# Kernel tuning notes

Measured on AMD Instinct MI355X. Metric: run time of the kernel, lower is better.

The kernel has to match this reference:

```python
import jax, jax.numpy as jnp
import numpy as np

B = 64
H = 768  # hidden_dim; x is [B, H, H], split along dim 1 into Q, D of [B, H//2, H]


def setup_inputs() -> dict:
    key = jax.random.key(0)
    kx, kw, kb = jax.random.split(key, 3)
    x = jax.random.normal(kx, (B, H, H), dtype=jnp.float32)
    # nn.Linear(H, H): weight [out, in], bias [out]
    W = jax.random.normal(kw, (H, H), dtype=jnp.float32) * (1.0 / np.sqrt(H))
    b = jax.random.normal(kb, (H,), dtype=jnp.float32) * 0.01
    return {"x": x, "W": W, "b": b}


def reference(x, W, b):
    T = H // 2
    Q = x[:, :T, :]          # [B, T, H]
    D = x[:, T:2 * T, :]     # [B, T, H]
    # Q = tanh(Linear(Q)); torch Linear: y = x @ W^T + b
    Q = jnp.tanh(jnp.einsum('bth,oh->bto', Q, W) + b)  # [B, T, H]
    D_t = jnp.swapaxes(D, 1, 2)                         # [B, H, T]
    L = jnp.einsum('bth,bsh->bts', Q, D)                # [B, T, T]
    A_Q = jnp.swapaxes(jax.nn.softmax(L, axis=1), 1, 2) # softmax over dim 1, then transpose -> [B, T, T]
    C_Q = jnp.matmul(D_t, A_Q)                          # [B, H, T]
    Q_t = jnp.swapaxes(Q, 1, 2)                         # [B, H, T]
    A_D = jax.nn.softmax(L, axis=2)                     # [B, T, T]
    C_D = jnp.matmul(jnp.concatenate((Q_t, C_Q), axis=1), A_D)  # [B, 2H, T]
    C_D_t = jnp.swapaxes(C_D, 1, 2)                     # [B, T, 2H]
    return jnp.concatenate((C_D_t, D), axis=2)          # [B, T, 3H]
```

## Files before the change

kernel.cpp:

```cpp
#include <hip/hip_runtime.h>


typedef __bf16 bf16x8 __attribute__((ext_vector_type(8)));
typedef __bf16 bf16x4 __attribute__((ext_vector_type(4)));
typedef float  f32x4  __attribute__((ext_vector_type(4)));

#define HH 768
#define TT 384

__device__ inline void split8(const float* __restrict__ p, bf16x8& hi, bf16x8& lo) {
    float4 f0 = *(const float4*)p;
    float4 f1 = *(const float4*)(p + 4);
    float f[8] = {f0.x, f0.y, f0.z, f0.w, f1.x, f1.y, f1.z, f1.w};
#pragma unroll
    for (int i = 0; i < 8; i++) {
        __bf16 h = (__bf16)f[i];
        hi[i] = h;
        lo[i] = (__bf16)(f[i] - (float)h);
    }
}

__device__ inline void split8r(float4 f0, float4 f1, bf16x8& hi, bf16x8& lo) {
    float f[8] = {f0.x, f0.y, f0.z, f0.w, f1.x, f1.y, f1.z, f1.w};
#pragma unroll
    for (int i = 0; i < 8; i++) {
        __bf16 h = (__bf16)f[i];
        hi[i] = h;
        lo[i] = (__bf16)(f[i] - (float)h);
    }
}

__device__ inline void gload16(const void* g, void* l) {
    __builtin_amdgcn_global_load_lds(
        (const __attribute__((address_space(1))) unsigned int*)g,
        (__attribute__((address_space(3))) unsigned int*)l, 16, 0, 0);
}

__global__ void prep_kernel(const float* __restrict__ x, __bf16* __restrict__ Dt,
                            float* __restrict__ out) {
    __shared__ float tile[32][33];
    int b = blockIdx.z;
    int h0 = blockIdx.x * 32, s0 = blockIdx.y * 32;
    int tx = threadIdx.x, ty = threadIdx.y;
    const float* src = x + ((size_t)b * HH + TT) * HH;
    float* outb = out + (size_t)b * TT * 2304;
#pragma unroll
    for (int j = 0; j < 4; j++) {
        int s = s0 + ty + 8 * j, h = h0 + tx;
        float v = src[(size_t)s * HH + h];
        tile[ty + 8 * j][tx] = v;
        outb[(size_t)s * 2304 + 1536 + h] = v;
    }
    __syncthreads();
    __bf16* Dtb = Dt + (size_t)b * HH * TT;
#pragma unroll
    for (int j = 0; j < 4; j++) {
        int h = h0 + ty + 8 * j, s = s0 + tx;
        Dtb[(size_t)h * TT + s] = (__bf16)tile[tx][ty + 8 * j];
    }
}

__global__ void splitW_kernel(const float* __restrict__ W, __bf16* __restrict__ Whi,
                              __bf16* __restrict__ Wlo) {
    int idx = blockIdx.x * 256 + threadIdx.x;
    bf16x8 h, l;
    split8(W + (size_t)idx * 8, h, l);
    *(bf16x8*)&Whi[(size_t)idx * 8] = h;
    *(bf16x8*)&Wlo[(size_t)idx * 8] = l;
}

__global__ __launch_bounds__(256) void gemm1_kernel(
    const float* __restrict__ x, const __bf16* __restrict__ Whi,
    const __bf16* __restrict__ Wlo, const float* __restrict__ bias,
    __bf16* __restrict__ Qhi, __bf16* __restrict__ Qlo, __bf16* __restrict__ M4) {
    __shared__ __bf16 Ah[128 * 32], Al[128 * 32];
    __shared__ __bf16 Bh[2][128 * 32], Bl[2][128 * 32];
    const int id = blockIdx.x;
    const int xcd = id & 7, kk = id >> 3;
    const int nb = kk % 6, p = (kk / 6) * 8 + xcd;
    const int mb = p % 3, b = p / 3;
    const int m_blk = mb * 128, n_blk = nb * 128;
    const int tid = threadIdx.x, lane = tid & 63, wave = tid >> 6;
    const int wm = wave >> 1, wn = wave & 1;
    const int r15 = lane & 15, quad = lane >> 4;
    const float* Abase = x + (size_t)b * HH * HH;
    const int ra0 = tid >> 2, qa = tid & 3;
    const float* aptr0 = Abase + (size_t)(m_blk + ra0) * HH + qa * 8;
    const float* aptr1 = Abase + (size_t)(m_blk + ra0 + 64) * HH + qa * 8;
    f32x4 acc[4][4];
#pragma unroll
    for (int i = 0; i < 4; i++)
#pragma unroll
        for (int j = 0; j < 4; j++) acc[i][j] = (f32x4){0.f, 0.f, 0.f, 0.f};

    float4 a00 = *(const float4*)(aptr0);
    float4 a01 = *(const float4*)(aptr0 + 4);
    float4 a10 = *(const float4*)(aptr1);
    float4 a11 = *(const float4*)(aptr1 + 4);
#pragma unroll
    for (int it = 0; it < 2; it++) {
        int c = it * 256 + tid, r = c >> 2, q = c & 3;
        gload16(Whi + (size_t)(n_blk + r) * HH + q * 8, &Bh[0][c * 8]);
        gload16(Wlo + (size_t)(n_blk + r) * HH + q * 8, &Bl[0][c * 8]);
    }
    int cur = 0;
    for (int k0 = 0; k0 < HH; k0 += 32) {
        {
            bf16x8 h, l;
            split8r(a00, a01, h, l);
            *(bf16x8*)&Ah[tid * 8] = h;
            *(bf16x8*)&Al[tid * 8] = l;
            split8r(a10, a11, h, l);
            *(bf16x8*)&Ah[(256 + tid) * 8] = h;
            *(bf16x8*)&Al[(256 + tid) * 8] = l;
        }
        __syncthreads();
        if (k0 + 32 < HH) {
            a00 = *(const float4*)(aptr0 + k0 + 32);
            a01 = *(const float4*)(aptr0 + k0 + 36);
            a10 = *(const float4*)(aptr1 + k0 + 32);
            a11 = *(const float4*)(aptr1 + k0 + 36);
#pragma unroll
            for (int it = 0; it < 2; it++) {
                int c = it * 256 + tid, r = c >> 2, q = c & 3;
                gload16(Whi + (size_t)(n_blk + r) * HH + k0 + 32 + q * 8, &Bh[cur ^ 1][c * 8]);
                gload16(Wlo + (size_t)(n_blk + r) * HH + k0 + 32 + q * 8, &Bl[cur ^ 1][c * 8]);
            }
        }
        bf16x8 ah[4], al[4], bh[4], bl[4];
#pragma unroll
        for (int i = 0; i < 4; i++) {
            int ra = (wm * 64 + i * 16 + r15) * 32 + quad * 8;
            ah[i] = *(const bf16x8*)&Ah[ra];
            al[i] = *(const bf16x8*)&Al[ra];
            int rb = (wn * 64 + i * 16 + r15) * 32 + quad * 8;
            bh[i] = *(const bf16x8*)&Bh[cur][rb];
            bl[i] = *(const bf16x8*)&Bl[cur][rb];
        }
#pragma unroll
        for (int i = 0; i < 4; i++)
#pragma unroll
            for (int j = 0; j < 4; j++) {
                acc[i][j] = __builtin_amdgcn_mfma_f32_16x16x32_bf16(ah[i], bh[j], acc[i][j], 0, 0, 0);
                acc[i][j] = __builtin_amdgcn_mfma_f32_16x16x32_bf16(ah[i], bl[j], acc[i][j], 0, 0, 0);
                acc[i][j] = __builtin_amdgcn_mfma_f32_16x16x32_bf16(al[i], bh[j], acc[i][j], 0, 0, 0);
            }
        __syncthreads();
        cur ^= 1;
    }
    __bf16* Qh = Qhi + (size_t)b * TT * HH;
    __bf16* Ql = Qlo + (size_t)b * TT * HH;
    __bf16* Mb = M4 + (size_t)b * 1536 * TT;
#pragma unroll
    for (int j = 0; j < 4; j++) {
        int col = n_blk + wn * 64 + j * 16 + r15;
        float bv = bias[col];
#pragma unroll
        for (int i = 0; i < 4; i++) {
            int row0 = m_blk + wm * 64 + i * 16 + quad * 4;
            bf16x4 mrow;
#pragma unroll
            for (int r = 0; r < 4; r++) {
                float v = tanhf(acc[i][j][r] + bv);
                __bf16 qh = (__bf16)v;
                Qh[(size_t)(row0 + r) * HH + col] = qh;
                Ql[(size_t)(row0 + r) * HH + col] = (__bf16)(v - (float)qh);
                mrow[r] = qh;
            }
            *(bf16x4*)&Mb[(size_t)col * TT + row0] = mrow;
        }
    }
}

__global__ __launch_bounds__(256) void gemm2_kernel(
    const __bf16* __restrict__ Qhi, const __bf16* __restrict__ Qlo,
    const float* __restrict__ x, float* __restrict__ L) {
    __shared__ __bf16 Ah[2][128 * 32], Al[2][128 * 32];
    __shared__ __bf16 Bh[128 * 32], Bl[128 * 32];
    const int id = blockIdx.x;
    const int xcd = id & 7, kk = id >> 3;
    const int inner = kk % 9, b = (kk / 9) * 8 + xcd;
    const int mb = inner / 3, nb = inner % 3;
    const int m_blk = mb * 128, n_blk = nb * 128;
    const int tid = threadIdx.x, lane = tid & 63, wave = tid >> 6;
    const int wm = wave >> 1, wn = wave & 1;
    const int r15 = lane & 15, quad = lane >> 4;
    const __bf16* Qh = Qhi + (size_t)b * TT * HH;
    const __bf16* Ql = Qlo + (size_t)b * TT * HH;
    const float* Dbase = x + ((size_t)b * HH + TT) * HH;
    const int rb0 = tid >> 2, qb = tid & 3;
    const float* dptr0 = Dbase + (size_t)(n_blk + rb0) * HH + qb * 8;
    const float* dptr1 = Dbase + (size_t)(n_blk + rb0 + 64) * HH + qb * 8;
    f32x4 acc[4][4];
#pragma unroll
    for (int i = 0; i < 4; i++)
#pragma unroll
        for (int j = 0; j < 4; j++) acc[i][j] = (f32x4){0.f, 0.f, 0.f, 0.f};

    float4 d00 = *(const float4*)(dptr0);
    float4 d01 = *(const float4*)(dptr0 + 4);
    float4 d10 = *(const float4*)(dptr1);
    float4 d11 = *(const float4*)(dptr1 + 4);
#pragma unroll
    for (int it = 0; it < 2; it++) {
        int c = it * 256 + tid, r = c >> 2, q = c & 3;
        gload16(Qh + (size_t)(m_blk + r) * HH + q * 8, &Ah[0][c * 8]);
        gload16(Ql + (size_t)(m_blk + r) * HH + q * 8, &Al[0][c * 8]);
    }
    int cur = 0;
    for (int k0 = 0; k0 < HH; k0 += 32) {
        {
            bf16x8 h, l;
            split8r(d00, d01, h, l);
            *(bf16x8*)&Bh[tid * 8] = h;
            *(bf16x8*)&Bl[tid * 8] = l;
            split8r(d10, d11, h, l);
            *(bf16x8*)&Bh[(256 + tid) * 8] = h;
            *(bf16x8*)&Bl[(256 + tid) * 8] = l;
        }
        __syncthreads();
        if (k0 + 32 < HH) {
            d00 = *(const float4*)(dptr0 + k0 + 32);
            d01 = *(const float4*)(dptr0 + k0 + 36);
            d10 = *(const float4*)(dptr1 + k0 + 32);
            d11 = *(const float4*)(dptr1 + k0 + 36);
#pragma unroll
            for (int it = 0; it < 2; it++) {
                int c = it * 256 + tid, r = c >> 2, q = c & 3;
                gload16(Qh + (size_t)(m_blk + r) * HH + k0 + 32 + q * 8, &Ah[cur ^ 1][c * 8]);
                gload16(Ql + (size_t)(m_blk + r) * HH + k0 + 32 + q * 8, &Al[cur ^ 1][c * 8]);
            }
        }
        bf16x8 ah[4], al[4], bh[4], bl[4];
#pragma unroll
        for (int i = 0; i < 4; i++) {
            int ra = (wm * 64 + i * 16 + r15) * 32 + quad * 8;
            ah[i] = *(const bf16x8*)&Ah[cur][ra];
            al[i] = *(const bf16x8*)&Al[cur][ra];
            int rb = (wn * 64 + i * 16 + r15) * 32 + quad * 8;
            bh[i] = *(const bf16x8*)&Bh[rb];
            bl[i] = *(const bf16x8*)&Bl[rb];
        }
#pragma unroll
        for (int i = 0; i < 4; i++)
#pragma unroll
            for (int j = 0; j < 4; j++) {
                acc[i][j] = __builtin_amdgcn_mfma_f32_16x16x32_bf16(ah[i], bh[j], acc[i][j], 0, 0, 0);
                acc[i][j] = __builtin_amdgcn_mfma_f32_16x16x32_bf16(ah[i], bl[j], acc[i][j], 0, 0, 0);
                acc[i][j] = __builtin_amdgcn_mfma_f32_16x16x32_bf16(al[i], bh[j], acc[i][j], 0, 0, 0);
            }
        __syncthreads();
        cur ^= 1;
    }
    float* Lb = L + (size_t)b * TT * TT;
#pragma unroll
    for (int j = 0; j < 4; j++) {
        int col = n_blk + wn * 64 + j * 16 + r15;
#pragma unroll
        for (int i = 0; i < 4; i++) {
            int row0 = m_blk + wm * 64 + i * 16 + quad * 4;
#pragma unroll
            for (int r = 0; r < 4; r++) Lb[(size_t)(row0 + r) * TT + col] = acc[i][j][r];
        }
    }
}

__global__ void softmax_col_kernel(const float* __restrict__ L, __bf16* __restrict__ AQt) {
    int b = blockIdx.y;
    int tx = threadIdx.x, ty = threadIdx.y;
    int s = blockIdx.x * 64 + tx;
    const float* Lb = L + (size_t)b * TT * TT;
    __shared__ float red[4][64];
    float mx = -1e30f;
    for (int t = ty; t < TT; t += 4) mx = fmaxf(mx, Lb[(size_t)t * TT + s]);
    red[ty][tx] = mx;
    __syncthreads();
    mx = fmaxf(fmaxf(red[0][tx], red[1][tx]), fmaxf(red[2][tx], red[3][tx]));
    float sum = 0.f;
    for (int t = ty; t < TT; t += 4) sum += __expf(Lb[(size_t)t * TT + s] - mx);
    __syncthreads();
    red[ty][tx] = sum;
    __syncthreads();
    float inv = 1.0f / (red[0][tx] + red[1][tx] + red[2][tx] + red[3][tx]);
    __bf16* Ab = AQt + (size_t)b * TT * TT;
    for (int t = ty; t < TT; t += 4)
        Ab[(size_t)t * TT + s] = (__bf16)(__expf(Lb[(size_t)t * TT + s] - mx) * inv);
}

__global__ void softmax_row_kernel(const float* __restrict__ L, __bf16* __restrict__ ADt) {
    int b = blockIdx.y;
    int t0 = blockIdx.x * 64;
    int tx = threadIdx.x, ty = threadIdx.y;
    int tid = ty * 64 + tx;
    const float* Lb = L + (size_t)b * TT * TT;
    __shared__ __bf16 ex[64][TT];
    for (int rr = ty; rr < 64; rr += 4) {
        const float* row = Lb + (size_t)(t0 + rr) * TT;
        float v[6];
        float mx = -1e30f;
#pragma unroll
        for (int k = 0; k < 6; k++) {
            v[k] = row[tx + 64 * k];
            mx = fmaxf(mx, v[k]);
        }
#pragma unroll
        for (int off = 32; off > 0; off >>= 1) mx = fmaxf(mx, __shfl_xor(mx, off));
        float sum = 0.f;
#pragma unroll
        for (int k = 0; k < 6; k++) {
            v[k] = __expf(v[k] - mx);
            sum += v[k];
        }
#pragma unroll
        for (int off = 32; off > 0; off >>= 1) sum += __shfl_xor(sum, off);
        float inv = 1.0f / sum;
#pragma unroll
        for (int k = 0; k < 6; k++) ex[rr][tx + 64 * k] = (__bf16)(v[k] * inv);
    }
    __syncthreads();
    __bf16* Ab = ADt + (size_t)b * TT * TT;
    for (int s = tid; s < TT; s += 256) {
#pragma unroll
        for (int j = 0; j < 8; j++) {
            bf16x8 t8;
#pragma unroll
            for (int e = 0; e < 8; e++) t8[e] = ex[j * 8 + e][s];
            *(bf16x8*)&Ab[(size_t)s * TT + t0 + j * 8] = t8;
        }
    }
}

__global__ __launch_bounds__(256) void gemm3_kernel(
    const __bf16* __restrict__ Dt, const __bf16* __restrict__ AQt,
    __bf16* __restrict__ M4) {
    __shared__ __bf16 As[128 * 32], Bs[128 * 32];
    const int id = blockIdx.x;
    const int xcd = id & 7, kk = id >> 3;
    const int inner = kk % 18, b = (kk / 18) * 8 + xcd;
    const int nb = inner % 3, mb = inner / 3;
    const int m_blk = mb * 128, n_blk = nb * 128;
    const int tid = threadIdx.x, lane = tid & 63, wave = tid >> 6;
    const int wm = wave >> 1, wn = wave & 1;
    const int r15 = lane & 15, quad = lane >> 4;
    const __bf16* Ab = Dt + (size_t)b * HH * TT;
    const __bf16* Bb = AQt + (size_t)b * TT * TT;
    f32x4 acc[4][4];
#pragma unroll
    for (int i = 0; i < 4; i++)
#pragma unroll
        for (int j = 0; j < 4; j++) acc[i][j] = (f32x4){0.f, 0.f, 0.f, 0.f};

    for (int k0 = 0; k0 < TT; k0 += 32) {
#pragma unroll
        for (int it = 0; it < 2; it++) {
            int c = it * 256 + tid;
            int r = c >> 2, q = c & 3;
            gload16(Ab + (size_t)(m_blk + r) * TT + k0 + q * 8, &As[c * 8]);
            gload16(Bb + (size_t)(n_blk + r) * TT + k0 + q * 8, &Bs[c * 8]);
        }
        __syncthreads();
        bf16x8 a[4], bf[4];
#pragma unroll
        for (int i = 0; i < 4; i++) {
            a[i] = *(const bf16x8*)&As[(wm * 64 + i * 16 + r15) * 32 + quad * 8];
            bf[i] = *(const bf16x8*)&Bs[(wn * 64 + i * 16 + r15) * 32 + quad * 8];
        }
#pragma unroll
        for (int i = 0; i < 4; i++)
#pragma unroll
            for (int j = 0; j < 4; j++)
                acc[i][j] = __builtin_amdgcn_mfma_f32_16x16x32_bf16(a[i], bf[j], acc[i][j], 0, 0, 0);
        __syncthreads();
    }
    __bf16* Mb = M4 + (size_t)b * 1536 * TT;
#pragma unroll
    for (int j = 0; j < 4; j++) {
        int col = n_blk + wn * 64 + j * 16 + r15;
#pragma unroll
        for (int i = 0; i < 4; i++) {
            int row0 = m_blk + wm * 64 + i * 16 + quad * 4;
#pragma unroll
            for (int r = 0; r < 4; r++)
                Mb[(size_t)(768 + row0 + r) * TT + col] = (__bf16)acc[i][j][r];
        }
    }
}

__global__ __launch_bounds__(256) void gemm4_kernel(
    const __bf16* __restrict__ ADt, const __bf16* __restrict__ M4,
    float* __restrict__ out) {
    __shared__ __bf16 As[128 * 32], Bs[128 * 32];
    const int id = blockIdx.x;
    const int xcd = id & 7, kk = id >> 3;
    const int inner = kk % 36, b = (kk / 36) * 8 + xcd;
    const int nb = inner % 12, mb = inner / 12;
    const int m_blk = mb * 128, n_blk = nb * 128;
    const int tid = threadIdx.x, lane = tid & 63, wave = tid >> 6;
    const int wm = wave >> 1, wn = wave & 1;
    const int r15 = lane & 15, quad = lane >> 4;
    const __bf16* Ab = ADt + (size_t)b * TT * TT;
    const __bf16* Bb = M4 + (size_t)b * 1536 * TT;
    f32x4 acc[4][4];
#pragma unroll
    for (int i = 0; i < 4; i++)
#pragma unroll
        for (int j = 0; j < 4; j++) acc[i][j] = (f32x4){0.f, 0.f, 0.f, 0.f};

    for (int k0 = 0; k0 < TT; k0 += 32) {
#pragma unroll
        for (int it = 0; it < 2; it++) {
            int c = it * 256 + tid;
            int r = c >> 2, q = c & 3;
            gload16(Ab + (size_t)(m_blk + r) * TT + k0 + q * 8, &As[c * 8]);
            gload16(Bb + (size_t)(n_blk + r) * TT + k0 + q * 8, &Bs[c * 8]);
        }
        __syncthreads();
        bf16x8 a[4], bf[4];
#pragma unroll
        for (int i = 0; i < 4; i++) {
            a[i] = *(const bf16x8*)&As[(wm * 64 + i * 16 + r15) * 32 + quad * 8];
            bf[i] = *(const bf16x8*)&Bs[(wn * 64 + i * 16 + r15) * 32 + quad * 8];
        }
#pragma unroll
        for (int i = 0; i < 4; i++)
#pragma unroll
            for (int j = 0; j < 4; j++)
                acc[i][j] = __builtin_amdgcn_mfma_f32_16x16x32_bf16(a[i], bf[j], acc[i][j], 0, 0, 0);
        __syncthreads();
    }
    float* outb = out + (size_t)b * TT * 2304;
#pragma unroll
    for (int j = 0; j < 4; j++) {
        int col = n_blk + wn * 64 + j * 16 + r15;
#pragma unroll
        for (int i = 0; i < 4; i++) {
            int row0 = m_blk + wm * 64 + i * 16 + quad * 4;
#pragma unroll
            for (int r = 0; r < 4; r++)
                outb[(size_t)(row0 + r) * 2304 + col] = acc[i][j][r];
        }
    }
}

extern "C" void kernel_launch(void* const* d_in, const int* in_sizes, int n_in,
                              void* d_out, int out_size, void* d_ws, size_t ws_size,
                              hipStream_t stream) {
    const float* x = (const float*)d_in[0];
    const float* W = (const float*)d_in[1];
    const float* bias = (const float*)d_in[2];
    float* out = (float*)d_out;
    char* ws = (char*)d_ws;

    __bf16* Qhi = (__bf16*)(ws + 0);
    __bf16* Qlo = (__bf16*)(ws + 37748736);
    __bf16* M4 = (__bf16*)(ws + 75497472);
    __bf16* Dt = (__bf16*)(ws + 150994944);
    float* L = (float*)(ws + 188743680);
    __bf16* AQt = (__bf16*)(ws + 0);
    __bf16* ADt = (__bf16*)(ws + 37748736);
    __bf16* Whi = (__bf16*)(ws + 188743680);
    __bf16* Wlo = Whi + 768 * 768;

    prep_kernel<<<dim3(24, 12, 64), dim3(32, 8), 0, stream>>>(x, Dt, out);
    splitW_kernel<<<288, 256, 0, stream>>>(W, Whi, Wlo);
    gemm1_kernel<<<1152, 256, 0, stream>>>(x, Whi, Wlo, bias, Qhi, Qlo, M4);
    gemm2_kernel<<<576, 256, 0, stream>>>(Qhi, Qlo, x, L);
    softmax_col_kernel<<<dim3(6, 64), dim3(64, 4), 0, stream>>>(L, AQt);
    softmax_row_kernel<<<dim3(6, 64), dim3(64, 4), 0, stream>>>(L, ADt);
    gemm3_kernel<<<1152, 256, 0, stream>>>(Dt, AQt, M4);
    gemm4_kernel<<<2304, 256, 0, stream>>>(ADt, M4, out);
}
```

Before: 753.0 us.

## Merge prep into gemm1 launch and fuse both softmax kernels

Folds the D-transpose/copy prep work into the gemm1 launch as extra blocks appended after the GEMM blocks. It also merges the column and row softmax kernels into one launch that dispatches on block index. Together these cut two kernel launches and let independent work share the GPU. The gemm1 block-to-XCD swizzle is dropped in favour of a plain linear mapping, and both kernels now use a larger unified shared buffer, which may lower occupancy for the small prep and softmax blocks.

```diff
diff --git a/kernel.cpp b/kernel.cpp
--- a/kernel.cpp
+++ b/kernel.cpp
@@ -34,30 +34,6 @@
     __builtin_amdgcn_global_load_lds(
         (const __attribute__((address_space(1))) unsigned int*)g,
         (__attribute__((address_space(3))) unsigned int*)l, 16, 0, 0);
-}
-
-__global__ void prep_kernel(const float* __restrict__ x, __bf16* __restrict__ Dt,
-                            float* __restrict__ out) {
-    __shared__ float tile[32][33];
-    int b = blockIdx.z;
-    int h0 = blockIdx.x * 32, s0 = blockIdx.y * 32;
-    int tx = threadIdx.x, ty = threadIdx.y;
-    const float* src = x + ((size_t)b * HH + TT) * HH;
-    float* outb = out + (size_t)b * TT * 2304;
-#pragma unroll
-    for (int j = 0; j < 4; j++) {
-        int s = s0 + ty + 8 * j, h = h0 + tx;
-        float v = src[(size_t)s * HH + h];
-        tile[ty + 8 * j][tx] = v;
-        outb[(size_t)s * 2304 + 1536 + h] = v;
-    }
-    __syncthreads();
-    __bf16* Dtb = Dt + (size_t)b * HH * TT;
-#pragma unroll
-    for (int j = 0; j < 4; j++) {
-        int h = h0 + ty + 8 * j, s = s0 + tx;
-        Dtb[(size_t)h * TT + s] = (__bf16)tile[tx][ty + 8 * j];
-    }
 }
 
 __global__ void splitW_kernel(const float* __restrict__ W, __bf16* __restrict__ Whi,
@@ -69,18 +45,45 @@
     *(bf16x8*)&Wlo[(size_t)idx * 8] = l;
 }
 
-__global__ __launch_bounds__(256) void gemm1_kernel(
+__global__ __launch_bounds__(256) void fused_g1prep_kernel(
     const float* __restrict__ x, const __bf16* __restrict__ Whi,
     const __bf16* __restrict__ Wlo, const float* __restrict__ bias,
-    __bf16* __restrict__ Qhi, __bf16* __restrict__ Qlo, __bf16* __restrict__ M4) {
-    __shared__ __bf16 Ah[128 * 32], Al[128 * 32];
-    __shared__ __bf16 Bh[2][128 * 32], Bl[2][128 * 32];
+    __bf16* __restrict__ Qhi, __bf16* __restrict__ Qlo, __bf16* __restrict__ M4,
+    __bf16* __restrict__ Dt, float* __restrict__ out) {
+    __shared__ __align__(16) char smem[49152];
+    const int tid = threadIdx.x;
+    if (blockIdx.x >= 1152) {
+        float (*tile)[33] = (float(*)[33])smem;
+        int pid = blockIdx.x - 1152;
+        int hb = pid % 24, sb = (pid / 24) % 12, b = pid / 288;
+        int h0 = hb * 32, s0 = sb * 32;
+        int tx = tid & 31, ty = tid >> 5;
+        const float* src = x + ((size_t)b * HH + TT) * HH;
+        float* outb = out + (size_t)b * TT * 2304;
+#pragma unroll
+        for (int j = 0; j < 4; j++) {
+            int s = s0 + ty + 8 * j, h = h0 + tx;
+            float v = src[(size_t)s * HH + h];
+            tile[ty + 8 * j][tx] = v;
+            outb[(size_t)s * 2304 + 1536 + h] = v;
+        }
+        __syncthreads();
+        __bf16* Dtb = Dt + (size_t)b * HH * TT;
+#pragma unroll
+        for (int j = 0; j < 4; j++) {
+            int h = h0 + ty + 8 * j, s = s0 + tx;
+            Dtb[(size_t)h * TT + s] = (__bf16)tile[tx][ty + 8 * j];
+        }
+        return;
+    }
+    __bf16* Ah = (__bf16*)smem;
+    __bf16* Al = (__bf16*)(smem + 8192);
+    __bf16* Bh0 = (__bf16*)(smem + 16384);
+    __bf16* Bl0 = (__bf16*)(smem + 32768);
     const int id = blockIdx.x;
-    const int xcd = id & 7, kk = id >> 3;
-    const int nb = kk % 6, p = (kk / 6) * 8 + xcd;
-    const int mb = p % 3, b = p / 3;
+    const int nb = id % 6, mb = (id / 6) % 3, b = id / 18;
     const int m_blk = mb * 128, n_blk = nb * 128;
-    const int tid = threadIdx.x, lane = tid & 63, wave = tid >> 6;
+    const int lane = tid & 63, wave = tid >> 6;
     const int wm = wave >> 1, wn = wave & 1;
     const int r15 = lane & 15, quad = lane >> 4;
     const float* Abase = x + (size_t)b * HH * HH;
@@ -100,8 +103,8 @@
 #pragma unroll
     for (int it = 0; it < 2; it++) {
         int c = it * 256 + tid, r = c >> 2, q = c & 3;
-        gload16(Whi + (size_t)(n_blk + r) * HH + q * 8, &Bh[0][c * 8]);
-        gload16(Wlo + (size_t)(n_blk + r) * HH + q * 8, &Bl[0][c * 8]);
+        gload16(Whi + (size_t)(n_blk + r) * HH + q * 8, Bh0 + c * 8);
+        gload16(Wlo + (size_t)(n_blk + r) * HH + q * 8, Bl0 + c * 8);
     }
     int cur = 0;
     for (int k0 = 0; k0 < HH; k0 += 32) {
@@ -123,8 +126,10 @@
 #pragma unroll
             for (int it = 0; it < 2; it++) {
                 int c = it * 256 + tid, r = c >> 2, q = c & 3;
-                gload16(Whi + (size_t)(n_blk + r) * HH + k0 + 32 + q * 8, &Bh[cur ^ 1][c * 8]);
-                gload16(Wlo + (size_t)(n_blk + r) * HH + k0 + 32 + q * 8, &Bl[cur ^ 1][c * 8]);
+                gload16(Whi + (size_t)(n_blk + r) * HH + k0 + 32 + q * 8,
+                        Bh0 + (cur ^ 1) * 4096 + c * 8);
+                gload16(Wlo + (size_t)(n_blk + r) * HH + k0 + 32 + q * 8,
+                        Bl0 + (cur ^ 1) * 4096 + c * 8);
             }
         }
         bf16x8 ah[4], al[4], bh[4], bl[4];
@@ -134,8 +139,8 @@
             ah[i] = *(const bf16x8*)&Ah[ra];
             al[i] = *(const bf16x8*)&Al[ra];
             int rb = (wn * 64 + i * 16 + r15) * 32 + quad * 8;
-            bh[i] = *(const bf16x8*)&Bh[cur][rb];
-            bl[i] = *(const bf16x8*)&Bl[cur][rb];
+            bh[i] = *(const bf16x8*)&Bh0[cur * 4096 + rb];
+            bl[i] = *(const bf16x8*)&Bl0[cur * 4096 + rb];
         }
 #pragma unroll
         for (int i = 0; i < 4; i++)
@@ -265,67 +270,66 @@
     }
 }
 
-__global__ void softmax_col_kernel(const float* __restrict__ L, __bf16* __restrict__ AQt) {
+__global__ void sm_fused_kernel(const float* __restrict__ L, __bf16* __restrict__ AQt,
+                                __bf16* __restrict__ ADt) {
+    __shared__ __align__(16) char smem[49152];
     int b = blockIdx.y;
     int tx = threadIdx.x, ty = threadIdx.y;
-    int s = blockIdx.x * 64 + tx;
     const float* Lb = L + (size_t)b * TT * TT;
-    __shared__ float red[4][64];
-    float mx = -1e30f;
-    for (int t = ty; t < TT; t += 4) mx = fmaxf(mx, Lb[(size_t)t * TT + s]);
-    red[ty][tx] = mx;
-    __syncthreads();
-    mx = fmaxf(fmaxf(red[0][tx], red[1][tx]), fmaxf(red[2][tx], red[3][tx]));
-    float sum = 0.f;
-    for (int t = ty; t < TT; t += 4) sum += __expf(Lb[(size_t)t * TT + s] - mx);
-    __syncthreads();
-    red[ty][tx] = sum;
-    __syncthreads();
-    float inv = 1.0f / (red[0][tx] + red[1][tx] + red[2][tx] + red[3][tx]);
-    __bf16* Ab = AQt + (size_t)b * TT * TT;
-    for (int t = ty; t < TT; t += 4)
-        Ab[(size_t)t * TT + s] = (__bf16)(__expf(Lb[(size_t)t * TT + s] - mx) * inv);
-}
-
-__global__ void softmax_row_kernel(const float* __restrict__ L, __bf16* __restrict__ ADt) {
-    int b = blockIdx.y;
-    int t0 = blockIdx.x * 64;
-    int tx = threadIdx.x, ty = threadIdx.y;
-    int tid = ty * 64 + tx;
-    const float* Lb = L + (size_t)b * TT * TT;
-    __shared__ __bf16 ex[64][TT];
-    for (int rr = ty; rr < 64; rr += 4) {
-        const float* row = Lb + (size_t)(t0 + rr) * TT;
-        float v[6];
+    if (blockIdx.x < 6) {
+        float (*red)[64] = (float(*)[64])smem;
+        int s = blockIdx.x * 64 + tx;
         float mx = -1e30f;
-#pragma unroll
-        for (int k = 0; k < 6; k++) {
-            v[k] = row[tx + 64 * k];
-            mx = fmaxf(mx, v[k]);
-        }
-#pragma unroll
-        for (int off = 32; off > 0; off >>= 1) mx = fmaxf(mx, __shfl_xor(mx, off));
+        for (int t = ty; t < TT; t += 4) mx = fmaxf(mx, Lb[(size_t)t * TT + s]);
+        red[ty][tx] = mx;
+        __syncthreads();
+        mx = fmaxf(fmaxf(red[0][tx], red[1][tx]), fmaxf(red[2][tx], red[3][tx]));
         float sum = 0.f;
-#pragma unroll
-        for (int k = 0; k < 6; k++) {
-            v[k] = __expf(v[k] - mx);
-            sum += v[k];
-        }
-#pragma unroll
-        for (int off = 32; off > 0; off >>= 1) sum += __shfl_xor(sum, off);
-        float inv = 1.0f / sum;
-#pragma unroll
-        for (int k = 0; k < 6; k++) ex[rr][tx + 64 * k] = (__bf16)(v[k] * inv);
-    }
-    __syncthreads();
-    __bf16* Ab = ADt + (size_t)b * TT * TT;
-    for (int s = tid; s < TT; s += 256) {
-#pragma unroll
-        for (int j = 0; j < 8; j++) {
-            bf16x8 t8;
-#pragma unroll
-            for (int e = 0; e < 8; e++) t8[e] = ex[j * 8 + e][s];
-            *(bf16x8*)&Ab[(size_t)s * TT + t0 + j * 8] = t8;
+        for (int t = ty; t < TT; t += 4) sum += __expf(Lb[(size_t)t * TT + s] - mx);
+        __syncthreads();
+        red[ty][tx] = sum;
+        __syncthreads();
+        float inv = 1.0f / (red[0][tx] + red[1][tx] + red[2][tx] + red[3][tx]);
+        __bf16* Ab = AQt + (size_t)b * TT * TT;
+        for (int t = ty; t < TT; t += 4)
+            Ab[(size_t)t * TT + s] = (__bf16)(__expf(Lb[(size_t)t * TT + s] - mx) * inv);
+    } else {
+        __bf16 (*ex)[TT] = (__bf16(*)[TT])smem;
+        int t0 = (blockIdx.x - 6) * 64;
+        int tid = ty * 64 + tx;
+        for (int rr = ty; rr < 64; rr += 4) {
+            const float* row = Lb + (size_t)(t0 + rr) * TT;
+            float v[6];
+            float mx = -1e30f;
+#pragma unroll
+            for (int k = 0; k < 6; k++) {
+                v[k] = row[tx + 64 * k];
+                mx = fmaxf(mx, v[k]);
+            }
+#pragma unroll
+            for (int off = 32; off > 0; off >>= 1) mx = fmaxf(mx, __shfl_xor(mx, off));
+            float sum = 0.f;
+#pragma unroll
+            for (int k = 0; k < 6; k++) {
+                v[k] = __expf(v[k] - mx);
+                sum += v[k];
+            }
+#pragma unroll
+            for (int off = 32; off > 0; off >>= 1) sum += __shfl_xor(sum, off);
+            float inv = 1.0f / sum;
+#pragma unroll
+            for (int k = 0; k < 6; k++) ex[rr][tx + 64 * k] = (__bf16)(v[k] * inv);
+        }
+        __syncthreads();
+        __bf16* Ab = ADt + (size_t)b * TT * TT;
+        for (int s = tid; s < TT; s += 256) {
+#pragma unroll
+            for (int j = 0; j < 8; j++) {
+                bf16x8 t8;
+#pragma unroll
+                for (int e = 0; e < 8; e++) t8[e] = ex[j * 8 + e][s];
+                *(bf16x8*)&Ab[(size_t)s * TT + t0 + j * 8] = t8;
+            }
         }
     }
 }
@@ -461,12 +465,10 @@
     __bf16* Whi = (__bf16*)(ws + 188743680);
     __bf16* Wlo = Whi + 768 * 768;
 
-    prep_kernel<<<dim3(24, 12, 64), dim3(32, 8), 0, stream>>>(x, Dt, out);
     splitW_kernel<<<288, 256, 0, stream>>>(W, Whi, Wlo);
-    gemm1_kernel<<<1152, 256, 0, stream>>>(x, Whi, Wlo, bias, Qhi, Qlo, M4);
+    fused_g1prep_kernel<<<19584, 256, 0, stream>>>(x, Whi, Wlo, bias, Qhi, Qlo, M4, Dt, out);
     gemm2_kernel<<<576, 256, 0, stream>>>(Qhi, Qlo, x, L);
-    softmax_col_kernel<<<dim3(6, 64), dim3(64, 4), 0, stream>>>(L, AQt);
-    softmax_row_kernel<<<dim3(6, 64), dim3(64, 4), 0, stream>>>(L, ADt);
+    sm_fused_kernel<<<dim3(12, 64), dim3(64, 4), 0, stream>>>(L, AQt, ADt);
     gemm3_kernel<<<1152, 256, 0, stream>>>(Dt, AQt, M4);
     gemm4_kernel<<<2304, 256, 0, stream>>>(ADt, M4, out);
 }
```

New measurement: 716.6 us, median of 2. -4.8%, faster.
